# Kernel tuning notes

Hardware: AMD Instinct MI355X
Metric: run time of the kernel (lower is better)

Reference implementation:

```python
import jax, jax.numpy as jnp
import numpy as np

BSZ, L, H, P = 8, 4096, 512, 256  # batch, seq len, features, complex state dim (conj_sym)
DT_MIN, DT_MAX = 1e-3, 1e-1


def setup_inputs() -> dict:
    key = jax.random.key(0)
    k_u, k_B, k_C, k_D, k_dt = jax.random.split(key, 5)
    u = jax.random.normal(k_u, (BSZ, L, H), dtype=jnp.float32)
    # HiPPO-like stable init for the diagonal state matrix
    Lambda_re = -0.5 * jnp.ones((P,), dtype=jnp.float32)
    Lambda_im = jnp.pi * jnp.arange(P, dtype=jnp.float32)
    # lecun-normal-ish scaling for real/imag parts of B (fan_in = H) and C (fan_in = P)
    B = jax.random.normal(k_B, (P, H, 2), dtype=jnp.float32) / jnp.sqrt(2.0 * H)
    C = jax.random.normal(k_C, (H, P, 2), dtype=jnp.float32) / jnp.sqrt(2.0 * P)
    D = jax.random.normal(k_D, (H,), dtype=jnp.float32)
    log_step = jax.random.uniform(k_dt, (P, 1), dtype=jnp.float32,
                                  minval=jnp.log(DT_MIN), maxval=jnp.log(DT_MAX))
    return {"u": u, "Lambda_re": Lambda_re, "Lambda_im": Lambda_im,
            "B": B, "C": C, "D": D, "log_step": log_step}


def _binop(q_i, q_j):
    """Associative binary operator for diagonal linear recurrence."""
    A_i, b_i = q_i
    A_j, b_j = q_j
    return (A_j * A_i, A_j * b_i + b_j)


def reference(u, Lambda_re, Lambda_im, B, C, D, log_step):
    # --- setup / discretization (zero-order hold) ---
    Lambda = (Lambda_re + 1j * Lambda_im).astype(jnp.complex64)      # (P,)
    B_tilde = (B[..., 0] + 1j * B[..., 1]).astype(jnp.complex64)     # (P,H)
    C_tilde = (C[..., 0] + 1j * C[..., 1]).astype(jnp.complex64)     # (H,P)
    step = jnp.exp(log_step[:, 0])                                   # (P,)
    Lambda_bar = jnp.exp(Lambda * step)                              # (P,)
    B_bar = ((Lambda_bar - 1.0) / Lambda)[:, None] * B_tilde         # (P,H)

    # --- parallel scan over the sequence (diagonal SSM) ---
    Bu = jnp.einsum('blh,ph->blp', u, B_bar)                         # (B,L,P) complex64
    Lam = jnp.broadcast_to(Lambda_bar, Bu.shape)                     # (B,L,P)
    _, xs = jax.lax.associative_scan(_binop, (Lam, Bu), axis=1)      # (B,L,P)

    # --- emissions (factor 2 from conjugate symmetry) + feedthrough ---
    ys = 2.0 * jnp.einsum('blp,hp->blh', xs, C_tilde).real + D * u   # (B,L,H)
    return jax.nn.gelu(ys)
```

## Files before the change

kernel.cpp:

```cpp
#include <hip/hip_runtime.h>
#include <cstdint>
#include <cstddef>

typedef unsigned short u16;
typedef short short8 __attribute__((ext_vector_type(8)));
typedef float floatx4 __attribute__((ext_vector_type(4)));

#define DEVINL __device__ __forceinline__

static constexpr int BSZ = 8, SEQL = 4096, H = 512, P = 256;
static constexpr int M = BSZ * SEQL;
static constexpr int KD = 512;
static constexpr int ND = 512;
static constexpr int CHUNK = 64;
static constexpr int NCH = SEQL / CHUNK;

DEVINL u16 f2bf(float f) {
  union { float f; unsigned u; } v; v.f = f;
  unsigned r = (v.u + 0x7fffu + ((v.u >> 16) & 1u)) >> 16;
  return (u16)r;
}
DEVINL float bf2f(u16 h) {
  union { unsigned u; float f; } v; v.u = ((unsigned)h) << 16; return v.f;
}

DEVINL void gload_lds16(const u16* g, u16* l) {
  __builtin_amdgcn_global_load_lds(
      (const __attribute__((address_space(1))) unsigned*)g,
      (__attribute__((address_space(3))) unsigned*)l, 16, 0, 0);
}

__global__ void setup_kernel(const float* __restrict__ Lre, const float* __restrict__ Lim,
                             const float* __restrict__ logstep,
                             float2* __restrict__ lam, float2* __restrict__ ffac) {
  int p = threadIdx.x;
  if (p >= P) return;
  float lr = Lre[p], li = Lim[p];
  float st = expf(logstep[p]);
  float mag = expf(lr * st);
  float ang = li * st;
  float cr = mag * cosf(ang);
  float ci = mag * sinf(ang);
  lam[p] = make_float2(cr, ci);
  float a = cr - 1.0f, b = ci;
  float den = lr * lr + li * li;
  float fr = (a * lr + b * li) / den;
  float fi = (b * lr - a * li) / den;
  ffac[p] = make_float2(fr, fi);
}

__global__ void bt1_kernel(const float2* __restrict__ Bin,
                           const float2* __restrict__ ffac,
                           u16* __restrict__ bt1) {
  int idx = blockIdx.x * 256 + threadIdx.x;
  int p = idx / H, h = idx % H;
  float2 bv = Bin[(size_t)p * H + h];
  float2 f = ffac[p];
  float br = f.x * bv.x - f.y * bv.y;
  float bi = f.x * bv.y + f.y * bv.x;
  bt1[(size_t)(2 * p) * H + h]     = f2bf(br);
  bt1[(size_t)(2 * p + 1) * H + h] = f2bf(bi);
}

__global__ void bt2_kernel(const float* __restrict__ Cin, u16* __restrict__ bt2) {
  int idx = blockIdx.x * 256 + threadIdx.x;
  float c = Cin[idx];
  float v = (idx & 1) ? -2.0f * c : 2.0f * c;
  bt2[idx] = f2bf(v);
}

__global__ void ucvt_kernel(const float4* __restrict__ uin, ushort4* __restrict__ ubf) {
  int idx = blockIdx.x * 256 + threadIdx.x;
  float4 f = uin[idx];
  ushort4 o;
  o.x = f2bf(f.x); o.y = f2bf(f.y); o.z = f2bf(f.z); o.w = f2bf(f.w);
  ubf[idx] = o;
}

template <int MODE>
__global__ __launch_bounds__(256, 4) void gemm_bt(const u16* __restrict__ A,
                                                  const u16* __restrict__ Bt,
                                                  u16* __restrict__ outBf,
                                                  float* __restrict__ outF,
                                                  const float* __restrict__ Dv,
                                                  const u16* __restrict__ ubf) {
  __shared__ u16 As[128 * 32];
  __shared__ u16 Bs[128 * 32];
  const int tid = threadIdx.x;
  const int bm = blockIdx.x, bn = blockIdx.y;
  const int wave = tid >> 6, lane = tid & 63;
  const int quad = lane >> 4, l16 = lane & 15;
  const int wm = (wave & 1) << 6, wn = (wave >> 1) << 6;

  floatx4 acc[4][4] = {};

  const u16* Ab = A + (size_t)bm * 128 * KD;
  const u16* Bb = Bt + (size_t)bn * 128 * KD;
  const int srow = tid >> 2;
  const int scol = (tid & 3) << 3;

  for (int k0 = 0; k0 < KD; k0 += 32) {
    __syncthreads();
    gload_lds16(Ab + (size_t)srow * KD + k0 + scol,        &As[tid * 8]);
    gload_lds16(Ab + (size_t)(srow + 64) * KD + k0 + scol, &As[2048 + tid * 8]);
    gload_lds16(Bb + (size_t)srow * KD + k0 + scol,        &Bs[tid * 8]);
    gload_lds16(Bb + (size_t)(srow + 64) * KD + k0 + scol, &Bs[2048 + tid * 8]);
    __syncthreads();

    short8 af[4], bf[4];
#pragma unroll
    for (int t = 0; t < 4; t++)
      af[t] = *(const short8*)&As[(wm + t * 16 + l16) * 32 + quad * 8];
#pragma unroll
    for (int t = 0; t < 4; t++)
      bf[t] = *(const short8*)&Bs[(wn + t * 16 + l16) * 32 + quad * 8];
#pragma unroll
    for (int tm = 0; tm < 4; tm++)
#pragma unroll
      for (int tn = 0; tn < 4; tn++)
        acc[tm][tn] = __builtin_amdgcn_mfma_f32_16x16x32_bf16(af[tm], bf[tn], acc[tm][tn], 0, 0, 0);
  }

  const int row_base = bm * 128 + wm + quad * 4;
  const int col_base = bn * 128 + wn + l16;
  float dv[4];
  if (MODE == 1) {
#pragma unroll
    for (int tn = 0; tn < 4; tn++) dv[tn] = Dv[col_base + tn * 16];
  }
#pragma unroll
  for (int tm = 0; tm < 4; tm++) {
#pragma unroll
    for (int tn = 0; tn < 4; tn++) {
      int n = col_base + tn * 16;
#pragma unroll
      for (int r = 0; r < 4; r++) {
        int m = row_base + tm * 16 + r;
        float v = acc[tm][tn][r];
        if (MODE == 0) {
          outBf[(size_t)m * ND + n] = f2bf(v);
        } else {
          float uv = bf2f(ubf[(size_t)m * ND + n]);
          float ys = v + dv[tn] * uv;
          float y3 = ys * ys * ys;
          float t = tanhf(0.7978845608028654f * (ys + 0.044715f * y3));
          outF[(size_t)m * ND + n] = 0.5f * ys * (1.0f + t);
        }
      }
    }
  }
}

__global__ __launch_bounds__(256) void scan_carry(const u16* __restrict__ Bu,
                                                  const float2* __restrict__ lam,
                                                  float2* __restrict__ carry) {
  int p = threadIdx.x;
  int c = blockIdx.x;
  int b = blockIdx.y;
  float2 lm = lam[p];
  float xr = 0.f, xi = 0.f;
  const u16* base = Bu + ((size_t)b * SEQL + (size_t)c * CHUNK) * 512 + 2 * p;
  for (int l = 0; l < CHUNK; l++) {
    unsigned w = *(const unsigned*)(base + (size_t)l * 512);
    float br = bf2f((u16)(w & 0xffffu));
    float bi = bf2f((u16)(w >> 16));
    float nr = lm.x * xr - lm.y * xi + br;
    float ni = lm.x * xi + lm.y * xr + bi;
    xr = nr; xi = ni;
  }
  carry[((size_t)b * NCH + c) * P + p] = make_float2(xr, xi);
}

__global__ __launch_bounds__(256) void scan_prefix(const float2* __restrict__ carry,
                                                   const float2* __restrict__ lam,
                                                   float2* __restrict__ prefix) {
  int p = threadIdx.x;
  int b = blockIdx.x;
  float2 lm = lam[p];
  float ar = lm.x, ai = lm.y;
  for (int i = 0; i < 6; i++) { float nr = ar * ar - ai * ai, ni = 2.f * ar * ai; ar = nr; ai = ni; }
  float pr = 0.f, pi = 0.f;
  for (int c = 0; c < NCH; c++) {
    prefix[((size_t)b * NCH + c) * P + p] = make_float2(pr, pi);
    float2 ca = carry[((size_t)b * NCH + c) * P + p];
    float nr = ar * pr - ai * pi + ca.x;
    float ni = ar * pi + ai * pr + ca.y;
    pr = nr; pi = ni;
  }
}

__global__ __launch_bounds__(256) void scan_apply(u16* __restrict__ Bu,
                                                  const float2* __restrict__ lam,
                                                  const float2* __restrict__ prefix) {
  int p = threadIdx.x;
  int c = blockIdx.x;
  int b = blockIdx.y;
  float2 lm = lam[p];
  float2 pf = prefix[((size_t)b * NCH + c) * P + p];
  float xr = pf.x, xi = pf.y;
  u16* base = Bu + ((size_t)b * SEQL + (size_t)c * CHUNK) * 512 + 2 * p;
  for (int l = 0; l < CHUNK; l++) {
    unsigned* addr = (unsigned*)(base + (size_t)l * 512);
    unsigned w = *addr;
    float br = bf2f((u16)(w & 0xffffu));
    float bi = bf2f((u16)(w >> 16));
    float nr = lm.x * xr - lm.y * xi + br;
    float ni = lm.x * xi + lm.y * xr + bi;
    xr = nr; xi = ni;
    *addr = (unsigned)f2bf(nr) | ((unsigned)f2bf(ni) << 16);
  }
}

extern "C" void kernel_launch(void* const* d_in, const int* in_sizes, int n_in,
                              void* d_out, int out_size, void* d_ws, size_t ws_size,
                              hipStream_t stream) {
  const float* u      = (const float*)d_in[0];
  const float* Lre    = (const float*)d_in[1];
  const float* Lim    = (const float*)d_in[2];
  const float* Bin    = (const float*)d_in[3];
  const float* Cin    = (const float*)d_in[4];
  const float* Dv     = (const float*)d_in[5];
  const float* lstep  = (const float*)d_in[6];
  float* out          = (float*)d_out;

  char* ws = (char*)d_ws;
  float2* lam    = (float2*)(ws + 0);
  float2* ffac   = (float2*)(ws + 2048);
  u16*    bt1    = (u16*)   (ws + 4096);
  u16*    bt2    = (u16*)   (ws + 528384);
  u16*    ubf    = (u16*)   (ws + 1052672);
  u16*    Bu     = (u16*)   (ws + 34607104);
  float2* carry  = (float2*)(ws + 68161536);
  float2* prefix = (float2*)(ws + 69210112);

  setup_kernel<<<1, 256, 0, stream>>>(Lre, Lim, lstep, lam, ffac);
  bt1_kernel<<<(P * H) / 256, 256, 0, stream>>>((const float2*)Bin, ffac, bt1);
  bt2_kernel<<<(H * P * 2) / 256, 256, 0, stream>>>(Cin, bt2);
  ucvt_kernel<<<(M * H / 4) / 256, 256, 0, stream>>>((const float4*)u, (ushort4*)ubf);

  gemm_bt<0><<<dim3(M / 128, ND / 128), 256, 0, stream>>>(ubf, bt1, Bu, nullptr, nullptr, nullptr);

  scan_carry <<<dim3(NCH, BSZ), 256, 0, stream>>>(Bu, lam, carry);
  scan_prefix<<<BSZ, 256, 0, stream>>>(carry, lam, prefix);
  scan_apply <<<dim3(NCH, BSZ), 256, 0, stream>>>(Bu, lam, prefix);

  gemm_bt<1><<<dim3(M / 128, ND / 128), 256, 0, stream>>>(Bu, bt2, nullptr, out, Dv, ubf);
}
```

Measured before the change: 217.3 us.

## Widen GEMM K-tile with XOR-swizzled LDS and fold prefix scan into apply

The GEMM now stages 64-wide K tiles in LDS, using an XOR swizzle on column groups to avoid bank conflicts, and runs two MFMA sub-steps per barrier pair. This halves the number of K-loop synchronizations. The scan chunk shrinks to 32, and the separate single-block-per-batch prefix kernel is removed. Each apply block now recomputes its own prefix by sequentially folding all earlier chunk carries. That saves a serial kernel launch but adds redundant work that grows with chunk index (up to 127 carry loads per block), and the doubled LDS footprint may reduce occupancy.

```diff
diff --git a/kernel.cpp b/kernel.cpp
--- a/kernel.cpp
+++ b/kernel.cpp
@@ -12,7 +12,7 @@
 static constexpr int M = BSZ * SEQL;
 static constexpr int KD = 512;
 static constexpr int ND = 512;
-static constexpr int CHUNK = 64;
+static constexpr int CHUNK = 32;
 static constexpr int NCH = SEQL / CHUNK;
 
 DEVINL u16 f2bf(float f) {
@@ -84,41 +84,48 @@
                                                   float* __restrict__ outF,
                                                   const float* __restrict__ Dv,
                                                   const u16* __restrict__ ubf) {
-  __shared__ u16 As[128 * 32];
-  __shared__ u16 Bs[128 * 32];
+  __shared__ u16 As[128 * 64];
+  __shared__ u16 Bs[128 * 64];
   const int tid = threadIdx.x;
   const int bm = blockIdx.x, bn = blockIdx.y;
   const int wave = tid >> 6, lane = tid & 63;
   const int quad = lane >> 4, l16 = lane & 15;
   const int wm = (wave & 1) << 6, wn = (wave >> 1) << 6;
+  const int r7 = l16 & 7;
 
   floatx4 acc[4][4] = {};
 
   const u16* Ab = A + (size_t)bm * 128 * KD;
   const u16* Bb = Bt + (size_t)bn * 128 * KD;
-  const int srow = tid >> 2;
-  const int scol = (tid & 3) << 3;
-
-  for (int k0 = 0; k0 < KD; k0 += 32) {
+  const int srow = tid >> 3;
+  const int scol = (((tid & 7) ^ ((tid >> 3) & 7)) << 3);
+
+  for (int k0 = 0; k0 < KD; k0 += 64) {
     __syncthreads();
-    gload_lds16(Ab + (size_t)srow * KD + k0 + scol,        &As[tid * 8]);
-    gload_lds16(Ab + (size_t)(srow + 64) * KD + k0 + scol, &As[2048 + tid * 8]);
-    gload_lds16(Bb + (size_t)srow * KD + k0 + scol,        &Bs[tid * 8]);
-    gload_lds16(Bb + (size_t)(srow + 64) * KD + k0 + scol, &Bs[2048 + tid * 8]);
+#pragma unroll
+    for (int j = 0; j < 4; j++)
+      gload_lds16(Ab + (size_t)(j * 32 + srow) * KD + k0 + scol, &As[j * 2048 + tid * 8]);
+#pragma unroll
+    for (int j = 0; j < 4; j++)
+      gload_lds16(Bb + (size_t)(j * 32 + srow) * KD + k0 + scol, &Bs[j * 2048 + tid * 8]);
     __syncthreads();
 
-    short8 af[4], bf[4];
-#pragma unroll
-    for (int t = 0; t < 4; t++)
-      af[t] = *(const short8*)&As[(wm + t * 16 + l16) * 32 + quad * 8];
-#pragma unroll
-    for (int t = 0; t < 4; t++)
-      bf[t] = *(const short8*)&Bs[(wn + t * 16 + l16) * 32 + quad * 8];
-#pragma unroll
-    for (int tm = 0; tm < 4; tm++)
-#pragma unroll
-      for (int tn = 0; tn < 4; tn++)
-        acc[tm][tn] = __builtin_amdgcn_mfma_f32_16x16x32_bf16(af[tm], bf[tn], acc[tm][tn], 0, 0, 0);
+#pragma unroll
+    for (int h = 0; h < 2; h++) {
+      const int pc = (((h << 2) | quad) ^ r7) << 3;
+      short8 af[4], bfr[4];
+#pragma unroll
+      for (int t = 0; t < 4; t++)
+        af[t] = *(const short8*)&As[(wm + t * 16 + l16) * 64 + pc];
+#pragma unroll
+      for (int t = 0; t < 4; t++)
+        bfr[t] = *(const short8*)&Bs[(wn + t * 16 + l16) * 64 + pc];
+#pragma unroll
+      for (int tm = 0; tm < 4; tm++)
+#pragma unroll
+        for (int tn = 0; tn < 4; tn++)
+          acc[tm][tn] = __builtin_amdgcn_mfma_f32_16x16x32_bf16(af[tm], bfr[tn], acc[tm][tn], 0, 0, 0);
+    }
   }
 
   const int row_base = bm * 128 + wm + quad * 4;
@@ -171,33 +178,23 @@
   carry[((size_t)b * NCH + c) * P + p] = make_float2(xr, xi);
 }
 
-__global__ __launch_bounds__(256) void scan_prefix(const float2* __restrict__ carry,
-                                                   const float2* __restrict__ lam,
-                                                   float2* __restrict__ prefix) {
-  int p = threadIdx.x;
-  int b = blockIdx.x;
-  float2 lm = lam[p];
-  float ar = lm.x, ai = lm.y;
-  for (int i = 0; i < 6; i++) { float nr = ar * ar - ai * ai, ni = 2.f * ar * ai; ar = nr; ai = ni; }
-  float pr = 0.f, pi = 0.f;
-  for (int c = 0; c < NCH; c++) {
-    prefix[((size_t)b * NCH + c) * P + p] = make_float2(pr, pi);
-    float2 ca = carry[((size_t)b * NCH + c) * P + p];
-    float nr = ar * pr - ai * pi + ca.x;
-    float ni = ar * pi + ai * pr + ca.y;
-    pr = nr; pi = ni;
-  }
-}
-
 __global__ __launch_bounds__(256) void scan_apply(u16* __restrict__ Bu,
                                                   const float2* __restrict__ lam,
-                                                  const float2* __restrict__ prefix) {
+                                                  const float2* __restrict__ carry) {
   int p = threadIdx.x;
   int c = blockIdx.x;
   int b = blockIdx.y;
   float2 lm = lam[p];
-  float2 pf = prefix[((size_t)b * NCH + c) * P + p];
-  float xr = pf.x, xi = pf.y;
+  float ar = lm.x, ai = lm.y;
+#pragma unroll
+  for (int i = 0; i < 5; i++) { float nr = ar * ar - ai * ai, ni = 2.f * ar * ai; ar = nr; ai = ni; }
+  float xr = 0.f, xi = 0.f;
+  for (int j = 0; j < c; j++) {
+    float2 ca = carry[((size_t)b * NCH + j) * P + p];
+    float nr = ar * xr - ai * xi + ca.x;
+    float ni = ar * xi + ai * xr + ca.y;
+    xr = nr; xi = ni;
+  }
   u16* base = Bu + ((size_t)b * SEQL + (size_t)c * CHUNK) * 512 + 2 * p;
   for (int l = 0; l < CHUNK; l++) {
     unsigned* addr = (unsigned*)(base + (size_t)l * 512);
@@ -231,7 +228,6 @@
   u16*    ubf    = (u16*)   (ws + 1052672);
   u16*    Bu     = (u16*)   (ws + 34607104);
   float2* carry  = (float2*)(ws + 68161536);
-  float2* prefix = (float2*)(ws + 69210112);
 
   setup_kernel<<<1, 256, 0, stream>>>(Lre, Lim, lstep, lam, ffac);
   bt1_kernel<<<(P * H) / 256, 256, 0, stream>>>((const float2*)Bin, ffac, bt1);
@@ -240,9 +236,8 @@
 
   gemm_bt<0><<<dim3(M / 128, ND / 128), 256, 0, stream>>>(ubf, bt1, Bu, nullptr, nullptr, nullptr);
 
-  scan_carry <<<dim3(NCH, BSZ), 256, 0, stream>>>(Bu, lam, carry);
-  scan_prefix<<<BSZ, 256, 0, stream>>>(carry, lam, prefix);
-  scan_apply <<<dim3(NCH, BSZ), 256, 0, stream>>>(Bu, lam, prefix);
+  scan_carry<<<dim3(NCH, BSZ), 256, 0, stream>>>(Bu, lam, carry);
+  scan_apply<<<dim3(NCH, BSZ), 256, 0, stream>>>(Bu, lam, carry);
 
   gemm_bt<1><<<dim3(M / 128, ND / 128), 256, 0, stream>>>(Bu, bt2, nullptr, out, Dv, ubf);
 }
```

Result: slower. 235.3 us (+8.3%).
